# Performance work log

Measured on AMD Instinct MI355X. Metric: run time of the kernel, lower is better.

## Reference

```python
import jax, jax.numpy as jnp
import numpy as np

KERNEL_SIZE = 5
SIGMA = 1.5
SIGMA_COLOR = 0.1
EPS = 1e-8


def _gaussian_kernel_2d(k, sigma):
    x = jnp.arange(k, dtype=jnp.float32) - k // 2
    k1 = jnp.exp(-0.5 * (x / sigma) ** 2)
    k1 = k1 / k1.sum()
    return jnp.outer(k1, k1)  # [k, k]


def setup_inputs() -> dict:
    key = jax.random.key(0)
    img = jax.random.uniform(key, (2, 3, 1024, 1024), dtype=jnp.float32)
    return {"img": img}


def reference(img):
    # Bilateral filter, faithful to Denoise._bilateral_filter.
    B, C, H, W = img.shape
    k = KERNEL_SIZE
    pad = k // 2
    k2 = _gaussian_kernel_2d(k, SIGMA).astype(img.dtype).reshape(-1)  # [k*k]

    img_padded = jnp.pad(img, ((0, 0), (0, 0), (pad, pad), (pad, pad)), mode='reflect')
    # patches: [B, C, H, W, k*k] via k*k shifted views (loop over fixed small window)
    patches = jnp.stack(
        [img_padded[:, :, i:i + H, j:j + W] for i in range(k) for j in range(k)],
        axis=-1,
    )
    center = img[..., None]
    intensity_diff = patches - center
    color_weights = jnp.exp(-0.5 * (intensity_diff / SIGMA_COLOR) ** 2)
    weights = color_weights * k2  # broadcast spatial gaussian over last axis
    weights_sum = weights.sum(axis=-1, keepdims=True) + EPS
    weights_normalized = weights / weights_sum
    img_filtered = (patches * weights_normalized).sum(axis=-1)
    return img_filtered
```

## Files before the change

kernel.cpp:

```cpp
#include <hip/hip_runtime.h>


#define TX 64
#define TY 64
#define BY 4
#define RPT (TY / BY)
#define PAD 2
#define LW (TX + 2 * PAD)
#define LH (TY + 2 * PAD)

typedef float f2 __attribute__((ext_vector_type(2)));

__device__ __forceinline__ f2 decode2(f2 t) {
    unsigned long long b = __builtin_bit_cast(unsigned long long, t);
    return __builtin_bit_cast(f2, b << 10);
}
__device__ __forceinline__ float decode1(float t) {
    return __builtin_bit_cast(float, __builtin_bit_cast(unsigned, t) << 10);
}

__global__ __launch_bounds__(256) void bilateral_kernel(
    const float* __restrict__ in, float* __restrict__ out, int H, int W)
{
    const int z  = blockIdx.z;
    const int x0 = blockIdx.x * TX;
    const int y0 = blockIdx.y * TY;
    const int tx = threadIdx.x;
    const int ty = threadIdx.y;
    const int tid = ty * TX + tx;

    const float S13  = 768.744433f;
    const float SEPS = 7.68744433e-6f;

    __shared__ float tile[LH * LW];
    const float* img = in + (size_t)z * H * W;

    for (int idx = tid; idx < LH * LW; idx += TX * BY) {
        int r = idx / LW;
        int c = idx - r * LW;
        int gy = y0 - PAD + r;
        int gx = x0 - PAD + c;
        gy = gy < 0 ? -gy : (gy >= H ? 2 * H - 2 - gy : gy);
        gx = gx < 0 ? -gx : (gx >= W ? 2 * W - 2 - gx : gx);
        tile[idx] = img[(size_t)gy * W + gx] * S13;
    }
    __syncthreads();

    constexpr double Ld[5] = {-3.0580100, -2.0962162, -1.7756103,
                              -2.0962162, -3.0580100};
    constexpr double A13   = 8192.0;
    constexpr double CMAG  = 12582912.0 + (127.0 - 0.043) * 8192.0;
#define CD(i, j) ((float)(CMAG + A13 * (Ld[i] + Ld[j])))

    const float K2C  = 0.0853118f;
    const float W22  = decode1(CD(2, 2));
    const float CORR = K2C - W22;

    const int ly0 = ty * RPT;

    f2    wA[6], wB[6];
    float wC[6];
#pragma unroll
    for (int r = 0; r < 4; ++r) {
        const int o = (ly0 + r) * LW + tx;
        wA[r] = f2{tile[o],     tile[o + 1]};
        wB[r] = f2{tile[o + 2], tile[o + 3]};
        wC[r] = tile[o + 4];
    }

#pragma unroll
    for (int q = 0; q < RPT; q += 2) {
        const int sA = (q + 4) % 6, sB = (q + 5) % 6;
        {
            const int o = (ly0 + q + 4) * LW + tx;
            wA[sA] = f2{tile[o], tile[o + 1]};
            wB[sA] = f2{tile[o + 2], tile[o + 3]};
            wC[sA] = tile[o + 4];
        }
        {
            const int o = (ly0 + q + 5) * LW + tx;
            wA[sB] = f2{tile[o], tile[o + 1]};
            wB[sB] = f2{tile[o + 2], tile[o + 3]};
            wC[sB] = tile[o + 4];
        }

        const float c0 = wB[(q + 2) % 6].x;
        const float c1 = wB[(q + 3) % 6].x;

        f2 ws0 = f2{CORR, 0.f},      vs0 = f2{CORR * c0, 0.f};
        f2 ws1 = f2{CORR, 0.f},      vs1 = f2{CORR * c1, 0.f};
        float wt0 = 0.f, vt0 = 0.f, wt1 = 0.f, vt1 = 0.f;

#pragma unroll
        for (int i = 0; i < 5; ++i) {
            const int r0 = (q + i) % 6;
            const int r1 = (q + 1 + i) % 6;
            const f2 CA = f2{CD(i, 0), CD(i, 1)};
            const f2 CB = f2{CD(i, 2), CD(i, 3)};
            const float C4 = CD(i, 4);
            {
                const f2 c2 = f2{c0, c0};
                f2 u = wA[r0] - c2;
                f2 w = decode2(__builtin_elementwise_fma(-u, u, CA));
                ws0 += w; vs0 = __builtin_elementwise_fma(w, wA[r0], vs0);
                u = wB[r0] - c2;
                w = decode2(__builtin_elementwise_fma(-u, u, CB));
                ws0 += w; vs0 = __builtin_elementwise_fma(w, wB[r0], vs0);
                const float us = wC[r0] - c0;
                const float wsc = decode1(__builtin_fmaf(-us, us, C4));
                wt0 += wsc; vt0 = __builtin_fmaf(wsc, wC[r0], vt0);
            }
            {
                const f2 c2 = f2{c1, c1};
                f2 u = wA[r1] - c2;
                f2 w = decode2(__builtin_elementwise_fma(-u, u, CA));
                ws1 += w; vs1 = __builtin_elementwise_fma(w, wA[r1], vs1);
                u = wB[r1] - c2;
                w = decode2(__builtin_elementwise_fma(-u, u, CB));
                ws1 += w; vs1 = __builtin_elementwise_fma(w, wB[r1], vs1);
                const float us = wC[r1] - c1;
                const float wsc = decode1(__builtin_fmaf(-us, us, C4));
                wt1 += wsc; vt1 = __builtin_fmaf(wsc, wC[r1], vt1);
            }
        }
        const float w0 = (ws0.x + ws0.y) + (wt0);
        const float v0 = (vs0.x + vs0.y) + (vt0);
        const float w1 = (ws1.x + ws1.y) + (wt1);
        const float v1 = (vs1.x + vs1.y) + (vt1);
        const float r0v = __builtin_amdgcn_rcpf(__builtin_fmaf(S13, w0, SEPS));
        const float r1v = __builtin_amdgcn_rcpf(__builtin_fmaf(S13, w1, SEPS));
        const size_t base = ((size_t)z * H + (y0 + ly0 + q)) * W + (x0 + tx);
        out[base]     = v0 * r0v;
        out[base + W] = v1 * r1v;
    }
#undef CD
}

extern "C" void kernel_launch(void* const* d_in, const int* in_sizes, int n_in,
                              void* d_out, int out_size, void* d_ws, size_t ws_size,
                              hipStream_t stream) {
    const float* img = (const float*)d_in[0];
    float* out = (float*)d_out;

    const int B = 2, C = 3, H = 1024, W = 1024;
    dim3 block(TX, BY, 1);
    dim3 grid(W / TX, H / TY, B * C);
    bilateral_kernel<<<grid, block, 0, stream>>>(img, out, H, W);
}
```

Measured before the change: 92.65 us.

## Pack fifth-column taps of two output rows into paired vector ops; halve tile height

Result: no change. 91.25 us (-1.5%).

```diff
diff --git a/kernel.cpp b/kernel.cpp
--- a/kernel.cpp
+++ b/kernel.cpp
@@ -2,7 +2,7 @@
 
 
 #define TX 64
-#define TY 64
+#define TY 32
 #define BY 4
 #define RPT (TY / BY)
 #define PAD 2
@@ -58,81 +58,93 @@
 
     const int ly0 = ty * RPT;
 
-    f2    wA[6], wB[6];
-    float wC[6];
+    f2 wA[6], wB[6], P[6];
+    {
+        float c4v[4];
 #pragma unroll
-    for (int r = 0; r < 4; ++r) {
-        const int o = (ly0 + r) * LW + tx;
-        wA[r] = f2{tile[o],     tile[o + 1]};
-        wB[r] = f2{tile[o + 2], tile[o + 3]};
-        wC[r] = tile[o + 4];
+        for (int r = 0; r < 4; ++r) {
+            const int o = (ly0 + r) * LW + tx;
+            wA[r]  = f2{tile[o],     tile[o + 1]};
+            wB[r]  = f2{tile[o + 2], tile[o + 3]};
+            c4v[r] = tile[o + 4];
+        }
+        P[0] = f2{c4v[0], c4v[1]};
+        P[1] = f2{c4v[1], c4v[2]};
+        P[2] = f2{c4v[2], c4v[3]};
     }
 
-#pragma unroll
-    for (int q = 0; q < RPT; q += 2) {
-        const int sA = (q + 4) % 6, sB = (q + 5) % 6;
-        {
-            const int o = (ly0 + q + 4) * LW + tx;
-            wA[sA] = f2{tile[o], tile[o + 1]};
-            wB[sA] = f2{tile[o + 2], tile[o + 3]};
-            wC[sA] = tile[o + 4];
-        }
-        {
-            const int o = (ly0 + q + 5) * LW + tx;
-            wA[sB] = f2{tile[o], tile[o + 1]};
-            wB[sB] = f2{tile[o + 2], tile[o + 3]};
-            wC[sB] = tile[o + 4];
-        }
+#define STEP(Q)                                                               \
+    {                                                                         \
+        float c4n, c5n;                                                       \
+        {                                                                     \
+            const int o = (ly0 + (Q) + 4) * LW + tx;                          \
+            wA[((Q) + 4) % 6] = f2{tile[o],     tile[o + 1]};                 \
+            wB[((Q) + 4) % 6] = f2{tile[o + 2], tile[o + 3]};                 \
+            c4n = tile[o + 4];                                                \
+        }                                                                     \
+        {                                                                     \
+            const int o = (ly0 + (Q) + 5) * LW + tx;                          \
+            wA[((Q) + 5) % 6] = f2{tile[o],     tile[o + 1]};                 \
+            wB[((Q) + 5) % 6] = f2{tile[o + 2], tile[o + 3]};                 \
+            c5n = tile[o + 4];                                                \
+        }                                                                     \
+        P[((Q) + 3) % 6] = f2{P[((Q) + 2) % 6].y, c4n};                       \
+        P[((Q) + 4) % 6] = f2{c4n, c5n};                                      \
+        const float c0 = wB[((Q) + 2) % 6].x;       \
+        const float c1 = wB[((Q) + 3) % 6].x;                                 \
+        const f2 cP = f2{c0, c1};                                             \
+        f2 ws0 = f2{CORR, 0.f}, vs0 = f2{CORR * c0, 0.f};                     \
+        f2 ws1 = f2{CORR, 0.f}, vs1 = f2{CORR * c1, 0.f};                     \
+        f2 wtP = f2{0.f, 0.f},  vtP = f2{0.f, 0.f};                           \
+        _Pragma("unroll")                                                     \
+        for (int i = 0; i < 5; ++i) {                                         \
+            const int r0 = ((Q) + i) % 6;                                     \
+            const int r1 = ((Q) + 1 + i) % 6;                                 \
+            const f2 CA = f2{CD(i, 0), CD(i, 1)};                             \
+            const f2 CB = f2{CD(i, 2), CD(i, 3)};                             \
+            const f2 C4 = f2{CD(i, 4), CD(i, 4)};                             \
+            {                             \
+                const f2 c2 = f2{c0, c0};                                     \
+                f2 u = wA[r0] - c2;                                           \
+                f2 w = decode2(__builtin_elementwise_fma(-u, u, CA));         \
+                ws0 += w; vs0 = __builtin_elementwise_fma(w, wA[r0], vs0);    \
+                u = wB[r0] - c2;                                              \
+                w = decode2(__builtin_elementwise_fma(-u, u, CB));            \
+                ws0 += w; vs0 = __builtin_elementwise_fma(w, wB[r0], vs0);    \
+            }                                                                 \
+            {                             \
+                const f2 c2 = f2{c1, c1};                                     \
+                f2 u = wA[r1] - c2;                                           \
+                f2 w = decode2(__builtin_elementwise_fma(-u, u, CA));         \
+                ws1 += w; vs1 = __builtin_elementwise_fma(w, wA[r1], vs1);    \
+                u = wB[r1] - c2;                                              \
+                w = decode2(__builtin_elementwise_fma(-u, u, CB));            \
+                ws1 += w; vs1 = __builtin_elementwise_fma(w, wB[r1], vs1);    \
+            }                                                                 \
+            {                      \
+                const f2 pv = P[r0];                                          \
+                f2 u = pv - cP;                                               \
+                f2 w = decode2(__builtin_elementwise_fma(-u, u, C4));         \
+                wtP += w; vtP = __builtin_elementwise_fma(w, pv, vtP);        \
+            }                                                                 \
+        }                                                                     \
+        const float w0 = (ws0.x + ws0.y) + wtP.x;                             \
+        const float v0 = (vs0.x + vs0.y) + vtP.x;                             \
+        const float w1 = (ws1.x + ws1.y) + wtP.y;                             \
+        const float v1 = (vs1.x + vs1.y) + vtP.y;                             \
+        const float r0v = __builtin_amdgcn_rcpf(__builtin_fmaf(S13, w0, SEPS)); \
+        const float r1v = __builtin_amdgcn_rcpf(__builtin_fmaf(S13, w1, SEPS)); \
+        const size_t base = ((size_t)z * H + (y0 + ly0 + (Q))) * W + (x0 + tx); \
+        out[base]     = v0 * r0v;                                             \
+        out[base + W] = v1 * r1v;                                             \
+    }
 
-        const float c0 = wB[(q + 2) % 6].x;
-        const float c1 = wB[(q + 3) % 6].x;
+    STEP(0)
+    STEP(2)
+    STEP(4)
+    STEP(6)
 
-        f2 ws0 = f2{CORR, 0.f},      vs0 = f2{CORR * c0, 0.f};
-        f2 ws1 = f2{CORR, 0.f},      vs1 = f2{CORR * c1, 0.f};
-        float wt0 = 0.f, vt0 = 0.f, wt1 = 0.f, vt1 = 0.f;
-
-#pragma unroll
-        for (int i = 0; i < 5; ++i) {
-            const int r0 = (q + i) % 6;
-            const int r1 = (q + 1 + i) % 6;
-            const f2 CA = f2{CD(i, 0), CD(i, 1)};
-            const f2 CB = f2{CD(i, 2), CD(i, 3)};
-            const float C4 = CD(i, 4);
-            {
-                const f2 c2 = f2{c0, c0};
-                f2 u = wA[r0] - c2;
-                f2 w = decode2(__builtin_elementwise_fma(-u, u, CA));
-                ws0 += w; vs0 = __builtin_elementwise_fma(w, wA[r0], vs0);
-                u = wB[r0] - c2;
-                w = decode2(__builtin_elementwise_fma(-u, u, CB));
-                ws0 += w; vs0 = __builtin_elementwise_fma(w, wB[r0], vs0);
-                const float us = wC[r0] - c0;
-                const float wsc = decode1(__builtin_fmaf(-us, us, C4));
-                wt0 += wsc; vt0 = __builtin_fmaf(wsc, wC[r0], vt0);
-            }
-            {
-                const f2 c2 = f2{c1, c1};
-                f2 u = wA[r1] - c2;
-                f2 w = decode2(__builtin_elementwise_fma(-u, u, CA));
-                ws1 += w; vs1 = __builtin_elementwise_fma(w, wA[r1], vs1);
-                u = wB[r1] - c2;
-                w = decode2(__builtin_elementwise_fma(-u, u, CB));
-                ws1 += w; vs1 = __builtin_elementwise_fma(w, wB[r1], vs1);
-                const float us = wC[r1] - c1;
-                const float wsc = decode1(__builtin_fmaf(-us, us, C4));
-                wt1 += wsc; vt1 = __builtin_fmaf(wsc, wC[r1], vt1);
-            }
-        }
-        const float w0 = (ws0.x + ws0.y) + (wt0);
-        const float v0 = (vs0.x + vs0.y) + (vt0);
-        const float w1 = (ws1.x + ws1.y) + (wt1);
-        const float v1 = (vs1.x + vs1.y) + (vt1);
-        const float r0v = __builtin_amdgcn_rcpf(__builtin_fmaf(S13, w0, SEPS));
-        const float r1v = __builtin_amdgcn_rcpf(__builtin_fmaf(S13, w1, SEPS));
-        const size_t base = ((size_t)z * H + (y0 + ly0 + q)) * W + (x0 + tx);
-        out[base]     = v0 * r0v;
-        out[base + W] = v1 * r1v;
-    }
+#undef STEP
 #undef CD
 }
 
```
